# Kernel optimization log

Hardware: AMD Instinct MI355X
Metric: run time of the kernel (lower is better)

Reference implementation:

```python
import jax, jax.numpy as jnp
import numpy as np

N_POINTS = 4_000_000   # total points in batch
N_PROPOSALS = 4096     # number of proposals
MIN_NPOINT = 256       # test_cfg.min_npoint: fixed slice length per proposal


def setup_inputs() -> dict:
    key = jax.random.key(0)
    k1, k2, k3 = jax.random.split(key, 3)
    semantic_scores = jax.random.normal(k1, (N_POINTS, 2), dtype=jnp.float32)
    pt_offsets = jax.random.normal(k2, (N_POINTS, 3), dtype=jnp.float32)
    # proposals_idx: column 0 = proposal id, column 1 = point index into [0, N)
    point_ids = jax.random.randint(k3, (N_PROPOSALS * MIN_NPOINT,), 0, N_POINTS, dtype=jnp.int32)
    prop_ids = jnp.repeat(jnp.arange(N_PROPOSALS, dtype=jnp.int32), MIN_NPOINT)
    proposals_idx = jnp.stack([prop_ids, point_ids], axis=1)  # [T, 2]
    # cumulative offsets; every proposal here has exactly MIN_NPOINT points
    proposals_offset = (jnp.arange(N_PROPOSALS + 1, dtype=jnp.int32) * MIN_NPOINT)
    return {
        "semantic_scores": semantic_scores,
        "proposals_offset": proposals_offset,
        "proposals_idx": proposals_idx,
        "pt_offsets": pt_offsets,
        "min_npoint": MIN_NPOINT,
    }


def reference(semantic_scores, proposals_offset, proposals_idx, pt_offsets, min_npoint):
    """Vectorized get_offset_4feats: per-proposal [mean, median, min, max] of
    ||pt_offsets[idx]|| over the first min_npoint indices of each proposal."""
    starts = proposals_offset[:-1]                                  # [P]
    gather = starts[:, None] + jnp.arange(min_npoint)[None, :]      # [P, K]
    prop_ind = proposals_idx[gather, 1]                             # [P, K] point indices
    radius = jnp.linalg.norm(pt_offsets[prop_ind], axis=-1)        # [P, K]
    srt = jnp.sort(radius, axis=1)                                  # one sort gives median/min/max
    mean = jnp.mean(radius, axis=1)
    median = srt[:, (min_npoint - 1) // 2]  # torch.median = lower middle for even K
    off_feats = jnp.stack([mean, median, srt[:, 0], srt[:, -1]], axis=1)  # [P, 4]
    return off_feats.astype(semantic_scores.dtype)
```

## Files before the change

### kernel.cpp

```cpp
#include <hip/hip_runtime.h>
#include <math.h>


#define CX_LANE(K, J)                                                         \
    {                                                                         \
        const int  ls       = (J) >> 2;                                       \
        const bool keep_min = (((e0 & (K)) == 0) == ((e0 & (J)) == 0));       \
        _Pragma("unroll")                                                     \
        for (int r = 0; r < 4; ++r) {                                         \
            const float o  = __shfl_xor(v[r], ls, 64);                        \
            const float mn = fminf(v[r], o);                                  \
            const float mx = fmaxf(v[r], o);                                  \
            v[r] = keep_min ? mn : mx;                                        \
        }                                                                     \
    }

#define CX_REG2(K)                                                            \
    {                                                                         \
        const bool a = ((e0 & (K)) == 0);                                     \
        float mn = fminf(v[0], v[2]), mx = fmaxf(v[0], v[2]);                 \
        v[0] = a ? mn : mx; v[2] = a ? mx : mn;                               \
        mn = fminf(v[1], v[3]); mx = fmaxf(v[1], v[3]);                       \
        v[1] = a ? mn : mx; v[3] = a ? mx : mn;                               \
    }

#define CX_REG1(K)                                                            \
    {                                                                         \
        const bool a01 = (((e0 + 0) & (K)) == 0);                             \
        const bool a23 = (((e0 + 2) & (K)) == 0);                             \
        float mn = fminf(v[0], v[1]), mx = fmaxf(v[0], v[1]);                 \
        v[0] = a01 ? mn : mx; v[1] = a01 ? mx : mn;                           \
        mn = fminf(v[2], v[3]); mx = fmaxf(v[2], v[3]);                       \
        v[2] = a23 ? mn : mx; v[3] = a23 ? mx : mn;                           \
    }

__global__ __launch_bounds__(256) void offs4feat_kernel(
    const int*   __restrict__ prop_offset,
    const int*   __restrict__ prop_idx,
    const float* __restrict__ pt_offsets,
    const int*   __restrict__ npoint_ptr,
    float*       __restrict__ out,
    int n_props)
{
    const int t    = threadIdx.x;
    const int lane = t & 63;
    const int p    = blockIdx.x * 4 + (t >> 6);
    if (p >= n_props) return;

    const int np    = *npoint_ptr;
    const int start = prop_offset[p];
    const int e0    = lane << 2;

    int id[4];
    if (e0 + 3 < np) {
        const int* base = prop_idx + (size_t)(start + e0) * 2;
        const int2 a = *(const int2*)(base + 0);
        const int2 b = *(const int2*)(base + 2);
        const int2 c = *(const int2*)(base + 4);
        const int2 d = *(const int2*)(base + 6);
        id[0] = a.y; id[1] = b.y; id[2] = c.y; id[3] = d.y;
    } else {
        #pragma unroll
        for (int r = 0; r < 4; ++r) {
            int ei = e0 + r; ei = (ei < np) ? ei : (np - 1);
            id[r] = prop_idx[(size_t)(start + ei) * 2 + 1];
        }
    }

    float x[4], y[4], z[4];
    #pragma unroll
    for (int r = 0; r < 4; ++r) {
        const float* q = pt_offsets + (size_t)id[r] * 3;
        x[r] = q[0]; y[r] = q[1]; z[r] = q[2];
    }

    float v[4];
    float s = 0.0f;
    #pragma unroll
    for (int r = 0; r < 4; ++r) {
        const float rr = sqrtf(fmaf(x[r], x[r], fmaf(y[r], y[r], z[r] * z[r])));
        const bool act = (e0 + r) < np;
        s   += act ? rr : 0.0f;
        v[r] = act ? rr : INFINITY;
    }

    #pragma unroll
    for (int o = 32; o > 0; o >>= 1) s += __shfl_xor(s, o, 64);

    CX_REG1(2)
    CX_REG2(4)  CX_REG1(4)
    CX_LANE(8, 4)   CX_REG2(8)   CX_REG1(8)
    CX_LANE(16, 8)  CX_LANE(16, 4)  CX_REG2(16)  CX_REG1(16)
    CX_LANE(32, 16) CX_LANE(32, 8)  CX_LANE(32, 4)  CX_REG2(32)  CX_REG1(32)
    CX_LANE(64, 32) CX_LANE(64, 16) CX_LANE(64, 8)  CX_LANE(64, 4)
    CX_REG2(64)  CX_REG1(64)
    CX_LANE(128, 64) CX_LANE(128, 32) CX_LANE(128, 16) CX_LANE(128, 8)
    CX_LANE(128, 4)  CX_REG2(128) CX_REG1(128)
    CX_LANE(256, 128) CX_LANE(256, 64) CX_LANE(256, 32) CX_LANE(256, 16)
    CX_LANE(256, 8)   CX_LANE(256, 4)  CX_REG2(256) CX_REG1(256)

    const int emed = (np - 1) >> 1;
    const int emax = np - 1;
    auto pick = [&](int rr_) {
        return rr_ == 0 ? v[0] : rr_ == 1 ? v[1] : rr_ == 2 ? v[2] : v[3];
    };
    if (lane == 0) {
        out[p * 4 + 0] = s / (float)np;
        out[p * 4 + 2] = v[0];
    }
    if (lane == (emed >> 2)) out[p * 4 + 1] = pick(emed & 3);
    if (lane == (emax >> 2)) out[p * 4 + 3] = pick(emax & 3);
}

extern "C" void kernel_launch(void* const* d_in, const int* in_sizes, int n_in,
                              void* d_out, int out_size, void* d_ws, size_t ws_size,
                              hipStream_t stream) {
    const int*   prop_offset = (const int*)  d_in[1];
    const int*   prop_idx    = (const int*)  d_in[2];
    const float* pt_offsets  = (const float*)d_in[3];
    const int*   npoint_ptr  = (const int*)  d_in[4];
    float*       out         = (float*)      d_out;

    const int n_proposals = in_sizes[1] - 1;
    const int n_blocks    = (n_proposals + 3) / 4;

    offs4feat_kernel<<<n_blocks, 256, 0, stream>>>(
        prop_offset, prop_idx, pt_offsets, npoint_ptr, out, n_proposals);
}
```

Baseline: 28.73 us.

## Precompute per-point radii in a workspace pass before gathering

Adds a streaming kernel that computes the norm of every point offset with float4 loads and writes a dense radius array into the workspace. The proposal kernel then gathers one float per index instead of three, shrinking the random-gather footprint. In exchange it streams and writes the entire point array, including points no proposal uses, and adds a second kernel launch. The old direct-gather path is kept as a fallback when the workspace is too small.

```diff
diff --git a/kernel.cpp b/kernel.cpp
--- a/kernel.cpp
+++ b/kernel.cpp
@@ -1,6 +1,32 @@
 #include <hip/hip_runtime.h>
 #include <math.h>
 
+
+__global__ __launch_bounds__(256) void radius_kernel(
+    const float* __restrict__ pts,
+    float*       __restrict__ rad,
+    int n_pts)
+{
+    const int q    = blockIdx.x * blockDim.x + threadIdx.x;
+    const int base = q * 4;
+    if (base + 3 < n_pts) {
+        const float4* f = (const float4*)(pts + (size_t)base * 3);
+        const float4 a = f[0], b = f[1], c = f[2];
+        float4 o;
+        o.x = sqrtf(fmaf(a.x, a.x, fmaf(a.y, a.y, a.z * a.z)));
+        o.y = sqrtf(fmaf(a.w, a.w, fmaf(b.x, b.x, b.y * b.y)));
+        o.z = sqrtf(fmaf(b.z, b.z, fmaf(b.w, b.w, c.x * c.x)));
+        o.w = sqrtf(fmaf(c.y, c.y, fmaf(c.z, c.z, c.w * c.w)));
+        *(float4*)(rad + base) = o;
+    } else if (base < n_pts) {
+        for (int i = base; i < n_pts; ++i) {
+            const float x = pts[(size_t)i * 3 + 0];
+            const float y = pts[(size_t)i * 3 + 1];
+            const float z = pts[(size_t)i * 3 + 2];
+            rad[i] = sqrtf(fmaf(x, x, fmaf(y, y, z * z)));
+        }
+    }
+}
 
 #define CX_LANE(K, J)                                                         \
     {                                                                         \
@@ -34,10 +60,11 @@
         v[2] = a23 ? mn : mx; v[3] = a23 ? mx : mn;                           \
     }
 
+template <int SRC>
 __global__ __launch_bounds__(256) void offs4feat_kernel(
     const int*   __restrict__ prop_offset,
     const int*   __restrict__ prop_idx,
-    const float* __restrict__ pt_offsets,
+    const float* __restrict__ src,
     const int*   __restrict__ npoint_ptr,
     float*       __restrict__ out,
     int n_props)
@@ -67,21 +94,26 @@
         }
     }
 
-    float x[4], y[4], z[4];
-    #pragma unroll
-    for (int r = 0; r < 4; ++r) {
-        const float* q = pt_offsets + (size_t)id[r] * 3;
-        x[r] = q[0]; y[r] = q[1]; z[r] = q[2];
+    float rr[4];
+    if (SRC == 0) {
+        #pragma unroll
+        for (int r = 0; r < 4; ++r) rr[r] = src[id[r]];
+    } else {
+        #pragma unroll
+        for (int r = 0; r < 4; ++r) {
+            const float* q = src + (size_t)id[r] * 3;
+            const float x = q[0], y = q[1], z = q[2];
+            rr[r] = sqrtf(fmaf(x, x, fmaf(y, y, z * z)));
+        }
     }
 
     float v[4];
     float s = 0.0f;
     #pragma unroll
     for (int r = 0; r < 4; ++r) {
-        const float rr = sqrtf(fmaf(x[r], x[r], fmaf(y[r], y[r], z[r] * z[r])));
         const bool act = (e0 + r) < np;
-        s   += act ? rr : 0.0f;
-        v[r] = act ? rr : INFINITY;
+        s   += act ? rr[r] : 0.0f;
+        v[r] = act ? rr[r] : INFINITY;
     }
 
     #pragma unroll
@@ -121,9 +153,18 @@
     const int*   npoint_ptr  = (const int*)  d_in[4];
     float*       out         = (float*)      d_out;
 
+    const int n_points    = in_sizes[3] / 3;
     const int n_proposals = in_sizes[1] - 1;
     const int n_blocks    = (n_proposals + 3) / 4;
 
-    offs4feat_kernel<<<n_blocks, 256, 0, stream>>>(
-        prop_offset, prop_idx, pt_offsets, npoint_ptr, out, n_proposals);
+    if (ws_size >= (size_t)n_points * sizeof(float)) {
+        float* radii = (float*)d_ws;
+        const int a_blocks = (n_points + 4 * 256 - 1) / (4 * 256);
+        radius_kernel<<<a_blocks, 256, 0, stream>>>(pt_offsets, radii, n_points);
+        offs4feat_kernel<0><<<n_blocks, 256, 0, stream>>>(
+            prop_offset, prop_idx, radii, npoint_ptr, out, n_proposals);
+    } else {
+        offs4feat_kernel<1><<<n_blocks, 256, 0, stream>>>(
+            prop_offset, prop_idx, pt_offsets, npoint_ptr, out, n_proposals);
+    }
 }
```

Measured after the change: 34.17 us. 1.19x slower.
